# Performance work log

Hardware: AMD Instinct MI355X
Metric: run time of the kernel (lower is better)

## Reference

```python
import jax, jax.numpy as jnp
import numpy as np

MULTI_INFER_NUM = 8
D_EMBED = 128
N_LAYERS = 2
T, B = 2048, 32


def setup_inputs() -> dict:
    key = jax.random.key(0)
    k1, k2, k3, k4 = jax.random.split(key, 4)
    positions = jax.random.randint(k1, (T, B), 0, 16, dtype=jnp.int64)
    outputs = jax.random.normal(k2, (T, B, D_EMBED), dtype=jnp.float32)
    # 4 LinearTransferFeatures per layer (self_forget, logit, logit_forget, out_forget)
    Ws = jax.random.normal(k3, (N_LAYERS, 4, MULTI_INFER_NUM + 1, D_EMBED, D_EMBED), dtype=jnp.float32) * 0.05
    bs = jax.random.normal(k4, (N_LAYERS, 4, MULTI_INFER_NUM + 1, D_EMBED), dtype=jnp.float32) * 0.05
    return {"positions": positions, "outputs": outputs, "Ws": Ws, "bs": bs}


def _linear(x, onehot, W, b):
    # x: [t,b,d]; onehot: [t,b,e]; W: [e,d,f]; b: [e,d]
    # Equivalent to gathering W[r_pos] ([t,b,d,f]) then einsum('ibde,ibd->ibe'),
    # but computed as per-expert GEMMs + one-hot combine (grouped-GEMM form).
    y_all = jnp.einsum('tbd,edf->tbef', x, W)      # per-expert outputs
    y = jnp.einsum('tbef,tbe->tbf', y_all, onehot)  # select token's expert
    return y + jnp.einsum('tbe,ed->tbd', onehot, b)


def reference(positions, outputs, Ws, bs):
    m = Ws.shape[2] - 1  # multi_infer_num
    r_pos = jnp.where(positions < m, positions, m)
    onehot = jax.nn.one_hot(r_pos, m + 1, dtype=outputs.dtype)
    x = outputs
    for l in range(Ws.shape[0]):
        self_forget = _linear(x, onehot, Ws[l, 0], bs[l, 0])
        logit = _linear(x, onehot, Ws[l, 1], bs[l, 1])
        logit_forget = _linear(x, onehot, Ws[l, 2], bs[l, 2])
        out_forget = _linear(x, onehot, Ws[l, 3], bs[l, 3])
        new_res = x * jax.nn.sigmoid(self_forget) + jnp.tanh(logit) * jax.nn.sigmoid(logit_forget)
        x = jnp.tanh(new_res) * jax.nn.sigmoid(out_forget)
    return x
```

## Files before the change

kernel.cpp:

```cpp
#include <hip/hip_runtime.h>
#include <hip/hip_fp16.h>
#include <stdint.h>

#define TOKENS 65536
#define D      128
#define NEXP   9
#define MT     32
#define MAXTILES (TOKENS / MT + NEXP)
#define NHB    256

typedef _Float16 f16;
typedef _Float16 f16x8  __attribute__((ext_vector_type(8)));
typedef float    f32x4  __attribute__((ext_vector_type(4)));
typedef uint32_t u32;

#define WI_TOKOFF  32
#define WI_TILEOFF 48
#define WI_HIST    128
#define WI_BBASE   2432
#define WI_PERM    4736
#define WS_WF_OFF  ((4736 + TOKENS) * 4)

#define LOG2E  1.44269504f
__device__ __forceinline__ float sigm(float v) {
  return __builtin_amdgcn_rcpf(1.0f + __builtin_amdgcn_exp2f(-LOG2E * v));
}
__device__ __forceinline__ float tanh_fast(float v) {
  return 1.0f - 2.0f * __builtin_amdgcn_rcpf(__builtin_amdgcn_exp2f(2.0f * LOG2E * v) + 1.0f);
}

__global__ void k_prep(const float* __restrict__ Ws, const int* __restrict__ pos,
                       int* __restrict__ wsI, f16* __restrict__ Wf) {
  const int tid = threadIdx.x;
  if (blockIdx.x < 288) {
    const int mat = blockIdx.x >> 2;
    const int q   = blockIdx.x & 3;
    const float* src = Ws + (size_t)mat * (D * D);
    f16* dst = Wf + (size_t)mat * (D * D);
#pragma unroll
    for (int p = 0; p < 2; ++p) {
      int cc = q * 512 + p * 256 + tid;
      int ln = cc & 63;
      int kb = (cc >> 6) & 3;
      int c  = cc >> 8;
      int quad = ln >> 4, n = ln & 15;
      int f  = c * 16 + n;
      int d0 = kb * 32 + quad * 8;
      f16x8 w;
#pragma unroll
      for (int i = 0; i < 8; ++i) w[i] = (f16)src[(d0 + i) * D + f];
      *(f16x8*)(dst + cc * 8) = w;
    }
  } else {
    const int b = blockIdx.x - 288;
    __shared__ int h[NEXP];
    if (tid < NEXP) h[tid] = 0;
    __syncthreads();
    int e = pos[b * 256 + tid]; e = e < 8 ? e : 8;
    atomicAdd(&h[e], 1);
    __syncthreads();
    if (tid < NEXP) wsI[WI_HIST + b * NEXP + tid] = h[tid];
  }
}

__global__ void k_scan(int* __restrict__ wsI) {
  const int tid = threadIdx.x;
  const int lane = tid & 63, w = tid >> 6;
  __shared__ int wsum[4];
  __shared__ int totalsS[NEXP];
  __shared__ int tokoffS[NEXP + 1];
  int rel[NEXP];
  int myh[NEXP];
#pragma unroll
  for (int e = 0; e < NEXP; ++e) myh[e] = wsI[WI_HIST + tid * NEXP + e];

  for (int e = 0; e < NEXP; ++e) {
    int v = myh[e];
    int x = v;
#pragma unroll
    for (int off = 1; off < 64; off <<= 1) {
      int y = __shfl_up(x, off);
      if (lane >= off) x += y;
    }
    if (lane == 63) wsum[w] = x;
    __syncthreads();
    int add = 0;
    for (int w2 = 0; w2 < w; ++w2) add += wsum[w2];
    int incl = x + add;
    rel[e] = incl - v;
    if (tid == 255) totalsS[e] = incl;
    __syncthreads();
  }
  if (tid == 0) {
    int tok = 0, tile = 0;
    wsI[WI_TOKOFF] = 0; wsI[WI_TILEOFF] = 0; tokoffS[0] = 0;
    for (int e = 0; e < NEXP; ++e) {
      int cnt = totalsS[e];
      tok += cnt; tile += (cnt + MT - 1) / MT;
      wsI[WI_TOKOFF + e + 1] = tok;  tokoffS[e + 1] = tok;
      wsI[WI_TILEOFF + e + 1] = tile;
    }
  }
  __syncthreads();
#pragma unroll
  for (int e = 0; e < NEXP; ++e)
    wsI[WI_BBASE + tid * NEXP + e] = tokoffS[e] + rel[e];
}

__global__ void k_assign(const int* __restrict__ pos, int* __restrict__ wsI) {
  const int tid = threadIdx.x, b = blockIdx.x;
  const int lane = tid & 63, w = tid >> 6;
  int e = pos[b * 256 + tid]; e = e < 8 ? e : 8;
  __shared__ int waveCnt[4][NEXP];
  __shared__ int waveBase[4][NEXP];
  int myRank = 0;
#pragma unroll
  for (int ee = 0; ee < NEXP; ++ee) {
    unsigned long long m = __ballot(e == ee);
    if (e == ee) myRank = __popcll(m & ((1ull << lane) - 1ull));
    if (lane == 0) waveCnt[w][ee] = __popcll(m);
  }
  __syncthreads();
  if (tid < NEXP) {
    int s = 0;
#pragma unroll
    for (int w2 = 0; w2 < 4; ++w2) { waveBase[w2][tid] = s; s += waveCnt[w2][tid]; }
  }
  __syncthreads();
  int base = wsI[WI_BBASE + b * NEXP + e];
  wsI[WI_PERM + base + waveBase[w][e] + myRank] = b * 256 + tid;
}

__launch_bounds__(256, 4)
__global__ void k_main(const float* __restrict__ xin, const float* __restrict__ bsPtr,
                       const int* __restrict__ wsI, const f16* __restrict__ Wf,
                       float* __restrict__ outPtr) {
  __shared__ __attribute__((aligned(16))) f16 Ash[MT][136];
  __shared__ int s_tok[MT];

  const int tid = threadIdx.x;
  const int bid = blockIdx.x;
  const int ntiles = wsI[WI_TILEOFF + NEXP];
  if (bid >= ntiles) return;

  int e = 0, tileOffE = 0;
#pragma unroll
  for (int ee = 0; ee < NEXP; ee++) {
    int to = wsI[WI_TILEOFF + ee];
    if (to <= bid) { e = ee; tileOffE = to; }
  }
  const int tokStart = wsI[WI_TOKOFF + e] + (bid - tileOffE) * MT;
  const int tokEnd   = wsI[WI_TOKOFF + e + 1];
  const int rowsValid = min(MT, tokEnd - tokStart);

  {
    int m = tid >> 3, h = tid & 7;
    bool valid = (m < rowsValid);
    int tok = 0;
    if (valid) tok = wsI[WI_PERM + tokStart + m];
    if (h == 0) s_tok[m] = valid ? tok : -1;
    const float4* src = (const float4*)(xin + (size_t)tok * D + h * 16);
    f16* drow = &Ash[m][h * 16];
#pragma unroll
    for (int i = 0; i < 2; i++) {
      float4 a = make_float4(0.f, 0.f, 0.f, 0.f), b2 = a;
      if (valid) { a = src[2 * i]; b2 = src[2 * i + 1]; }
      f16x8 wv;
      wv[0] = (f16)a.x;  wv[1] = (f16)a.y;  wv[2] = (f16)a.z;  wv[3] = (f16)a.w;
      wv[4] = (f16)b2.x; wv[5] = (f16)b2.y; wv[6] = (f16)b2.z; wv[7] = (f16)b2.w;
      *(f16x8*)&drow[i * 8] = wv;
    }
  }
  __syncthreads();

  const int lane = tid & 63;
  const int n    = lane & 15;
  const int quad = lane >> 4;
  const int cBase = (tid >> 6) * 2;
  const int vlane = lane * 8;
  const f16* We = Wf + (size_t)e * 16384;

  f16x8 aF0[4], aF1[4];
  f16x8 b0[4], b1[4];
  f32x4 acc[4][2];

#define LOAD_AF()                                                              \
  do {                                                                         \
    _Pragma("unroll")                                                          \
    for (int _kb = 0; _kb < 4; ++_kb) {                                        \
      aF0[_kb] = *(const f16x8*)&Ash[n][_kb * 32 + quad * 8];                  \
      aF1[_kb] = *(const f16x8*)&Ash[16 + n][_kb * 32 + quad * 8];             \
    }                                                                          \
  } while (0)

#define PREFETCH_B(BUF, LL, CC, JJ)                                            \
  do {                                                                         \
    if ((LL) < 2) {                                                            \
      const f16* _p = We + ((LL) * 4 + (JJ)) * 147456 + (CC) * 2048 + vlane;   \
      _Pragma("unroll")                                                        \
      for (int _kb = 0; _kb < 4; ++_kb)                                        \
        BUF[_kb] = *(const f16x8*)(_p + _kb * 512);                            \
    }                                                                          \
  } while (0)

#define MFMA2(G, BUF)                                                          \
  do {                                                                         \
    f32x4 _x = {0.f, 0.f, 0.f, 0.f}, _y = {0.f, 0.f, 0.f, 0.f};                \
    _Pragma("unroll")                                                          \
    for (int _kb = 0; _kb < 4; ++_kb) {                                        \
      _x = __builtin_amdgcn_mfma_f32_16x16x32_f16(aF0[_kb], BUF[_kb], _x, 0, 0, 0); \
      _y = __builtin_amdgcn_mfma_f32_16x16x32_f16(aF1[_kb], BUF[_kb], _y, 0, 0, 0); \
    }                                                                          \
    acc[G][0] = _x; acc[G][1] = _y;                                            \
  } while (0)

  PREFETCH_B(b0, 0, cBase, 0);
  LOAD_AF();
  __syncthreads();

#pragma unroll 1
  for (int l = 0; l < 2; l++) {
#pragma unroll 1
    for (int ci = 0; ci < 2; ci++) {
      const int cc = cBase + ci;
      const int f = cc * 16 + n;
      float bias[4];
#pragma unroll
      for (int j = 0; j < 4; j++)
        bias[j] = bsPtr[((l * 4 + j) * NEXP + e) * D + f];

      const int ln = (ci == 1) ? l + 1 : l;
      const int cn = (ci == 1) ? cBase : cc + 1;

      PREFETCH_B(b1, l, cc, 1);  MFMA2(0, b0);
      PREFETCH_B(b0, l, cc, 2);  MFMA2(1, b1);
      PREFETCH_B(b1, l, cc, 3);  MFMA2(2, b0);
      PREFETCH_B(b0, ln, cn, 0); MFMA2(3, b1);

#pragma unroll
      for (int s = 0; s < 2; s++) {
#pragma unroll
        for (int r = 0; r < 4; r++) {
          int m = s * 16 + quad * 4 + r;
          float sf = acc[0][s][r] + bias[0];
          float lg = acc[1][s][r] + bias[1];
          float lf = acc[2][s][r] + bias[2];
          float of = acc[3][s][r] + bias[3];
          float xv = (float)Ash[m][f];
          float nr = xv * sigm(sf) + tanh_fast(lg) * sigm(lf);
          float xn = tanh_fast(nr) * sigm(of);
          if (l == 0) {
            Ash[m][f] = (f16)xn;
          } else {
            int tok = s_tok[m];
            if (tok >= 0) outPtr[(size_t)tok * D + f] = xn;
          }
        }
      }
    }
    if (l == 0) {
      __syncthreads();
      LOAD_AF();
    }
  }
#undef LOAD_AF
#undef PREFETCH_B
#undef MFMA2
}

extern "C" void kernel_launch(void* const* d_in, const int* in_sizes, int n_in,
                              void* d_out, int out_size, void* d_ws, size_t ws_size,
                              hipStream_t stream) {
  const int*   pos = (const int*)d_in[0];
  const float* x   = (const float*)d_in[1];
  const float* Ws  = (const float*)d_in[2];
  const float* bs  = (const float*)d_in[3];
  float* out = (float*)d_out;
  int* wsI = (int*)d_ws;
  f16* Wf = (f16*)((char*)d_ws + WS_WF_OFF);

  k_prep  <<<544, 256, 0, stream>>>(Ws, pos, wsI, Wf);
  k_scan  <<<1, 256, 0, stream>>>(wsI);
  k_assign<<<NHB, 256, 0, stream>>>(pos, wsI);
  k_main  <<<MAXTILES, 256, 0, stream>>>(x, bs, wsI, Wf, out);
}
```

Measured before the change: 133.7 us.

## Pack sorted tokens into unpadded tiles with per-expert masked passes

Removes per-expert tile padding: the grid becomes exactly TOKENS/MT tiles over the sorted permutation, and a tile that straddles an expert boundary runs one masked pass per expert present. The intent is to drop the partially filled padding tiles and their zero-row work, and to simplify tile-to-expert lookup. It also raises launch bounds from 4 to 8 blocks per CU for occupancy, which risks register pressure or spills given the large MFMA fragment and accumulator state. Boundary tiles repeat the GEMM work once per extra expert.

```diff
diff --git a/kernel.cpp b/kernel.cpp
--- a/kernel.cpp
+++ b/kernel.cpp
@@ -6,16 +6,16 @@
 #define D      128
 #define NEXP   9
 #define MT     32
-#define MAXTILES (TOKENS / MT + NEXP)
+#define NTILES (TOKENS / MT)
 #define NHB    256
 
 typedef _Float16 f16;
 typedef _Float16 f16x8  __attribute__((ext_vector_type(8)));
 typedef float    f32x4  __attribute__((ext_vector_type(4)));
 typedef uint32_t u32;
+typedef unsigned long long u64;
 
 #define WI_TOKOFF  32
-#define WI_TILEOFF 48
 #define WI_HIST    128
 #define WI_BBASE   2432
 #define WI_PERM    4736
@@ -92,13 +92,11 @@
     __syncthreads();
   }
   if (tid == 0) {
-    int tok = 0, tile = 0;
-    wsI[WI_TOKOFF] = 0; wsI[WI_TILEOFF] = 0; tokoffS[0] = 0;
+    int tok = 0;
+    wsI[WI_TOKOFF] = 0; tokoffS[0] = 0;
     for (int e = 0; e < NEXP; ++e) {
-      int cnt = totalsS[e];
-      tok += cnt; tile += (cnt + MT - 1) / MT;
+      tok += totalsS[e];
       wsI[WI_TOKOFF + e + 1] = tok;  tokoffS[e + 1] = tok;
-      wsI[WI_TILEOFF + e + 1] = tile;
     }
   }
   __syncthreads();
@@ -116,7 +114,7 @@
   int myRank = 0;
 #pragma unroll
   for (int ee = 0; ee < NEXP; ++ee) {
-    unsigned long long m = __ballot(e == ee);
+    u64 m = __ballot(e == ee);
     if (e == ee) myRank = __popcll(m & ((1ull << lane) - 1ull));
     if (lane == 0) waveCnt[w][ee] = __popcll(m);
   }
@@ -131,40 +129,43 @@
   wsI[WI_PERM + base + waveBase[w][e] + myRank] = b * 256 + tid;
 }
 
-__launch_bounds__(256, 4)
+__launch_bounds__(256, 8)
 __global__ void k_main(const float* __restrict__ xin, const float* __restrict__ bsPtr,
                        const int* __restrict__ wsI, const f16* __restrict__ Wf,
                        float* __restrict__ outPtr) {
   __shared__ __attribute__((aligned(16))) f16 Ash[MT][136];
   __shared__ int s_tok[MT];
+  __shared__ int s_e[MT];
+  __shared__ int s_list[NEXP];
+  __shared__ int s_npass;
 
   const int tid = threadIdx.x;
   const int bid = blockIdx.x;
-  const int ntiles = wsI[WI_TILEOFF + NEXP];
-  if (bid >= ntiles) return;
-
-  int e = 0, tileOffE = 0;
-#pragma unroll
-  for (int ee = 0; ee < NEXP; ee++) {
-    int to = wsI[WI_TILEOFF + ee];
-    if (to <= bid) { e = ee; tileOffE = to; }
-  }
-  const int tokStart = wsI[WI_TOKOFF + e] + (bid - tileOffE) * MT;
-  const int tokEnd   = wsI[WI_TOKOFF + e + 1];
-  const int rowsValid = min(MT, tokEnd - tokStart);
+  const int lane = tid & 63;
+
+  if (tid < 64) {
+    int mm = lane & 31;
+    int row = bid * MT + mm;
+    int tok0 = wsI[WI_PERM + row];
+    int ee = 0;
+#pragma unroll
+    for (int k = 1; k < NEXP; ++k) ee += (row >= wsI[WI_TOKOFF + k]);
+    if (lane < 32) { s_tok[mm] = tok0; s_e[mm] = ee; }
+    int eprev = __shfl_up(ee, 1);
+    bool newrun = (lane < 32) && (lane == 0 || ee != eprev);
+    u64 runs = __ballot(newrun);
+    if (newrun) s_list[__popcll(runs & ((1ull << lane) - 1ull))] = ee;
+    if (lane == 0) s_npass = (int)__popcll(runs);
+  }
 
   {
     int m = tid >> 3, h = tid & 7;
-    bool valid = (m < rowsValid);
-    int tok = 0;
-    if (valid) tok = wsI[WI_PERM + tokStart + m];
-    if (h == 0) s_tok[m] = valid ? tok : -1;
+    int tok = wsI[WI_PERM + bid * MT + m];
     const float4* src = (const float4*)(xin + (size_t)tok * D + h * 16);
     f16* drow = &Ash[m][h * 16];
 #pragma unroll
     for (int i = 0; i < 2; i++) {
-      float4 a = make_float4(0.f, 0.f, 0.f, 0.f), b2 = a;
-      if (valid) { a = src[2 * i]; b2 = src[2 * i + 1]; }
+      float4 a = src[2 * i], b2 = src[2 * i + 1];
       f16x8 wv;
       wv[0] = (f16)a.x;  wv[1] = (f16)a.y;  wv[2] = (f16)a.z;  wv[3] = (f16)a.w;
       wv[4] = (f16)b2.x; wv[5] = (f16)b2.y; wv[6] = (f16)b2.z; wv[7] = (f16)b2.w;
@@ -173,12 +174,11 @@
   }
   __syncthreads();
 
-  const int lane = tid & 63;
   const int n    = lane & 15;
   const int quad = lane >> 4;
   const int cBase = (tid >> 6) * 2;
   const int vlane = lane * 8;
-  const f16* We = Wf + (size_t)e * 16384;
+  const int npass = __builtin_amdgcn_readfirstlane(s_npass);
 
   f16x8 aF0[4], aF1[4];
   f16x8 b0[4], b1[4];
@@ -214,53 +214,62 @@
     acc[G][0] = _x; acc[G][1] = _y;                                            \
   } while (0)
 
-  PREFETCH_B(b0, 0, cBase, 0);
-  LOAD_AF();
-  __syncthreads();
-
 #pragma unroll 1
-  for (int l = 0; l < 2; l++) {
+  for (int p = 0; p < npass; ++p) {
+    const int E = __builtin_amdgcn_readfirstlane(s_list[p]);
+    const f16* We = Wf + (size_t)E * 16384;
+    const u32 rowmask = (u32)__ballot(lane < 32 && s_e[lane] == E);
+    const u32 mybits = rowmask >> (quad * 4);
+
+    LOAD_AF();
+    PREFETCH_B(b0, 0, cBase, 0);
+    __syncthreads();
+
 #pragma unroll 1
-    for (int ci = 0; ci < 2; ci++) {
-      const int cc = cBase + ci;
-      const int f = cc * 16 + n;
-      float bias[4];
-#pragma unroll
-      for (int j = 0; j < 4; j++)
-        bias[j] = bsPtr[((l * 4 + j) * NEXP + e) * D + f];
-
-      const int ln = (ci == 1) ? l + 1 : l;
-      const int cn = (ci == 1) ? cBase : cc + 1;
-
-      PREFETCH_B(b1, l, cc, 1);  MFMA2(0, b0);
-      PREFETCH_B(b0, l, cc, 2);  MFMA2(1, b1);
-      PREFETCH_B(b1, l, cc, 3);  MFMA2(2, b0);
-      PREFETCH_B(b0, ln, cn, 0); MFMA2(3, b1);
-
-#pragma unroll
-      for (int s = 0; s < 2; s++) {
-#pragma unroll
-        for (int r = 0; r < 4; r++) {
-          int m = s * 16 + quad * 4 + r;
-          float sf = acc[0][s][r] + bias[0];
-          float lg = acc[1][s][r] + bias[1];
-          float lf = acc[2][s][r] + bias[2];
-          float of = acc[3][s][r] + bias[3];
-          float xv = (float)Ash[m][f];
-          float nr = xv * sigm(sf) + tanh_fast(lg) * sigm(lf);
-          float xn = tanh_fast(nr) * sigm(of);
-          if (l == 0) {
-            Ash[m][f] = (f16)xn;
-          } else {
-            int tok = s_tok[m];
-            if (tok >= 0) outPtr[(size_t)tok * D + f] = xn;
+    for (int l = 0; l < 2; l++) {
+#pragma unroll 1
+      for (int ci = 0; ci < 2; ci++) {
+        const int cc = cBase + ci;
+        const int f = cc * 16 + n;
+        float bias[4];
+#pragma unroll
+        for (int j = 0; j < 4; j++)
+          bias[j] = bsPtr[((l * 4 + j) * NEXP + E) * D + f];
+
+        const int ln = (ci == 1) ? l + 1 : l;
+        const int cn = (ci == 1) ? cBase : cc + 1;
+
+        PREFETCH_B(b1, l, cc, 1);  MFMA2(0, b0);
+        PREFETCH_B(b0, l, cc, 2);  MFMA2(1, b1);
+        PREFETCH_B(b1, l, cc, 3);  MFMA2(2, b0);
+        PREFETCH_B(b0, ln, cn, 0); MFMA2(3, b1);
+
+#pragma unroll
+        for (int s = 0; s < 2; s++) {
+#pragma unroll
+          for (int r = 0; r < 4; r++) {
+            int m = s * 16 + quad * 4 + r;
+            float sf = acc[0][s][r] + bias[0];
+            float lg = acc[1][s][r] + bias[1];
+            float lf = acc[2][s][r] + bias[2];
+            float of = acc[3][s][r] + bias[3];
+            float xv = (float)Ash[m][f];
+            float nr = xv * sigm(sf) + tanh_fast(lg) * sigm(lf);
+            float xn = tanh_fast(nr) * sigm(of);
+            if ((mybits >> (s * 16 + r)) & 1) {
+              if (l == 0) {
+                Ash[m][f] = (f16)xn;
+              } else {
+                outPtr[(size_t)s_tok[m] * D + f] = xn;
+              }
+            }
           }
         }
       }
-    }
-    if (l == 0) {
-      __syncthreads();
-      LOAD_AF();
+      if (l == 0) {
+        __syncthreads();
+        LOAD_AF();
+      }
     }
   }
 #undef LOAD_AF
@@ -282,5 +291,5 @@
   k_prep  <<<544, 256, 0, stream>>>(Ws, pos, wsI, Wf);
   k_scan  <<<1, 256, 0, stream>>>(wsI);
   k_assign<<<NHB, 256, 0, stream>>>(pos, wsI);
-  k_main  <<<MAXTILES, 256, 0, stream>>>(x, bs, wsI, Wf, out);
-}
+  k_main  <<<NTILES, 256, 0, stream>>>(x, bs, wsI, Wf, out);
+}
```

New measurement: 312.1 us. +133.5%, slower.
